# Optimization experiments

Hardware: AMD Instinct MI355X
Metric: run time of the kernel (lower is better)

The kernel has to match this reference:

```python
import jax, jax.numpy as jnp
import numpy as np

N, M, D = 8192, 8192, 1024

def setup_inputs() -> dict:
    key = jax.random.key(0)
    k1, k2 = jax.random.split(key)
    encoder_outputs = jax.random.normal(k1, (N, D), dtype=jnp.float32)
    fact_emb = jax.random.normal(k2, (M, D), dtype=jnp.float32)
    return {"encoder_outputs": encoder_outputs, "fact_emb": fact_emb}

def reference(encoder_outputs, fact_emb):
    # energy: [N, M] = encoder_outputs @ fact_emb^T (unscaled)
    energy = jnp.einsum('nd,md->nm', encoder_outputs, fact_emb)
    weights = jax.nn.softmax(energy, axis=1)          # softmax over facts
    outputs = jnp.einsum('nm,md->nd', weights, fact_emb)
    return (outputs, weights)
```

## Files before the change

kernel.cpp:

```cpp
#include <hip/hip_runtime.h>
#include <hip/hip_bf16.h>
#include <math.h>
#include <stdint.h>

#define N_ROWS 8192
#define M_FACTS 8192
#define D_DIM 1024

typedef __bf16 bf16x8_t __attribute__((ext_vector_type(8)));
typedef __bf16 bf16x4_t __attribute__((ext_vector_type(4)));
typedef float f32x4_t __attribute__((ext_vector_type(4)));

#define BM 128
#define BN 128
#define BK 32
#define PADK 40

__device__ __forceinline__ void gload_lds16(const void* g, void* lds) {
  __builtin_amdgcn_global_load_lds(
      (__attribute__((address_space(1))) void*)(uintptr_t)g,
      (__attribute__((address_space(3))) void*)(uint32_t)(uintptr_t)lds,
      16, 0, 0);
}


__global__ __launch_bounds__(256) void split_hi_lo(const float* __restrict__ X,
                                                   __bf16* __restrict__ H,
                                                   __bf16* __restrict__ L) {
  int i = blockIdx.x * 256 + threadIdx.x;
  float4 v = ((const float4*)X)[i];
  float f[4] = {v.x, v.y, v.z, v.w};
  bf16x4_t h, l;
#pragma unroll
  for (int q = 0; q < 4; q++) {
    __bf16 hh = (__bf16)f[q];
    h[q] = hh;
    l[q] = (__bf16)(f[q] - (float)hh);
  }
  ((bf16x4_t*)H)[i] = h;
  ((bf16x4_t*)L)[i] = l;
}

__global__ __launch_bounds__(256) void transpose_f_bf16(const float* __restrict__ F,
                                                        __bf16* __restrict__ Ft) {
  __shared__ float t[64 * 69];
  const int tid = threadIdx.x;
  const int m0 = blockIdx.x * 64, d0 = blockIdx.y * 64;
#pragma unroll
  for (int p = 0; p < 4; p++) {
    int flat = p * 256 + tid;
    int m = flat >> 4, dq = flat & 15;
    float4 v = *(const float4*)(F + (size_t)(m0 + m) * D_DIM + d0 + dq * 4);
    t[(dq * 4 + 0) * 69 + m] = v.x;
    t[(dq * 4 + 1) * 69 + m] = v.y;
    t[(dq * 4 + 2) * 69 + m] = v.z;
    t[(dq * 4 + 3) * 69 + m] = v.w;
  }
  __syncthreads();
#pragma unroll
  for (int q = 0; q < 2; q++) {
    int id = q * 256 + tid;
    int d = id >> 3, c = id & 7;
    const float* row = t + d * 69 + c * 8;
    bf16x8_t o;
#pragma unroll
    for (int i = 0; i < 8; i++) o[i] = (__bf16)row[i];
    *(bf16x8_t*)(Ft + (size_t)(d0 + d) * M_FACTS + m0 + c * 8) = o;
  }
}

__global__ __launch_bounds__(256) void gemm1_fast(const __bf16* __restrict__ Eh,
                                                  const __bf16* __restrict__ El,
                                                  const __bf16* __restrict__ Fh,
                                                  const __bf16* __restrict__ Fl,
                                                  float* __restrict__ C,
                                                  int row_base) {
  __shared__ __bf16 sAh[BM * BK], sAl[BM * BK], sBh[BN * BK], sBl[BN * BK];
  const int tid = threadIdx.x;
  const int wave = tid >> 6, lane = tid & 63;
  const int row0 = row_base + blockIdx.x * BM, col0 = blockIdx.y * BN;
  const int wm = wave >> 1, wn = wave & 1;
  const int lrow = lane & 15, quad = lane >> 4;

  f32x4_t acc[4][4];
#pragma unroll
  for (int i = 0; i < 4; i++)
#pragma unroll
    for (int j = 0; j < 4; j++) acc[i][j] = (f32x4_t){0.f, 0.f, 0.f, 0.f};

  for (int k0 = 0; k0 < D_DIM; k0 += BK) {
#pragma unroll
    for (int r = 0; r < 2; r++) {
      int c = (r * 4 + wave) * 64 + lane;
      int row = c >> 2;
      int ko = (c & 3) << 3;
      size_t ga = (size_t)(row0 + row) * D_DIM + k0 + ko;
      size_t gb = (size_t)(col0 + row) * D_DIM + k0 + ko;
      gload_lds16(Eh + ga, sAh + c * 8);
      gload_lds16(El + ga, sAl + c * 8);
      gload_lds16(Fh + gb, sBh + c * 8);
      gload_lds16(Fl + gb, sBl + c * 8);
    }
    __syncthreads();

    bf16x8_t ah[4], al[4], bh[4], bl[4];
#pragma unroll
    for (int i = 0; i < 4; i++) {
      int ra = (wm * 64 + i * 16 + lrow) * BK + quad * 8;
      ah[i] = *(const bf16x8_t*)(sAh + ra);
      al[i] = *(const bf16x8_t*)(sAl + ra);
      int rb = (wn * 64 + i * 16 + lrow) * BK + quad * 8;
      bh[i] = *(const bf16x8_t*)(sBh + rb);
      bl[i] = *(const bf16x8_t*)(sBl + rb);
    }
#pragma unroll
    for (int i = 0; i < 4; i++)
#pragma unroll
      for (int j = 0; j < 4; j++) {
        acc[i][j] = __builtin_amdgcn_mfma_f32_16x16x32_bf16(ah[i], bh[j], acc[i][j], 0, 0, 0);
        acc[i][j] = __builtin_amdgcn_mfma_f32_16x16x32_bf16(ah[i], bl[j], acc[i][j], 0, 0, 0);
        acc[i][j] = __builtin_amdgcn_mfma_f32_16x16x32_bf16(al[i], bh[j], acc[i][j], 0, 0, 0);
      }
    __syncthreads();
  }

#pragma unroll
  for (int i = 0; i < 4; i++) {
    int rbase = row0 + wm * 64 + i * 16 + quad * 4;
#pragma unroll
    for (int j = 0; j < 4; j++) {
      int c = col0 + wn * 64 + j * 16 + lrow;
#pragma unroll
      for (int r = 0; r < 4; r++) C[(size_t)(rbase + r) * M_FACTS + c] = acc[i][j][r];
    }
  }
}

__global__ __launch_bounds__(256) void gemm2_reg(const __bf16* __restrict__ Wb,
                                                 const __bf16* __restrict__ Ft,
                                                 float* __restrict__ O,
                                                 int out_row0) {
  __shared__ __bf16 sW[2][BM * BK];
  __shared__ __bf16 sF[2][BN * BK];
  const int tid = threadIdx.x;
  const int wave = tid >> 6, lane = tid & 63;
  const int row0 = blockIdx.x * BM;
  const int col0 = blockIdx.y * BN;
  const int wm = wave >> 1, wn = wave & 1;
  const int lrow = lane & 15, quad = lane >> 4;

  const int id0 = wave * 64 + lane;
  const int r0 = id0 >> 2, c0 = (id0 & 3) << 3;
  const int id1 = id0 + 256;
  const int r1 = id1 >> 2, c1 = (id1 & 3) << 3;

  const __bf16* gW = Wb + (size_t)row0 * M_FACTS;
  const __bf16* gF = Ft + (size_t)col0 * M_FACTS;

  f32x4_t acc[4][4];
#pragma unroll
  for (int i = 0; i < 4; i++)
#pragma unroll
    for (int j = 0; j < 4; j++) acc[i][j] = (f32x4_t){0.f, 0.f, 0.f, 0.f};

  bf16x8_t rW0, rW1, rF0, rF1;
  rW0 = *(const bf16x8_t*)(gW + (size_t)r0 * M_FACTS + c0);
  rW1 = *(const bf16x8_t*)(gW + (size_t)r1 * M_FACTS + c1);
  rF0 = *(const bf16x8_t*)(gF + (size_t)r0 * M_FACTS + c0);
  rF1 = *(const bf16x8_t*)(gF + (size_t)r1 * M_FACTS + c1);
  *(bf16x8_t*)(&sW[0][id0 * 8]) = rW0;
  *(bf16x8_t*)(&sW[0][id1 * 8]) = rW1;
  *(bf16x8_t*)(&sF[0][id0 * 8]) = rF0;
  *(bf16x8_t*)(&sF[0][id1 * 8]) = rF1;
  rW0 = *(const bf16x8_t*)(gW + (size_t)r0 * M_FACTS + BK + c0);
  rW1 = *(const bf16x8_t*)(gW + (size_t)r1 * M_FACTS + BK + c1);
  rF0 = *(const bf16x8_t*)(gF + (size_t)r0 * M_FACTS + BK + c0);
  rF1 = *(const bf16x8_t*)(gF + (size_t)r1 * M_FACTS + BK + c1);
  __syncthreads();

  const int NT = M_FACTS / BK;
  for (int it = 0; it < NT; it++) {
    const int cur = it & 1;
    bf16x8_t a[4], b[4];
#pragma unroll
    for (int i = 0; i < 4; i++) {
      a[i] = *(const bf16x8_t*)(&sW[cur][(wm * 64 + i * 16 + lrow) * BK + quad * 8]);
      b[i] = *(const bf16x8_t*)(&sF[cur][(wn * 64 + i * 16 + lrow) * BK + quad * 8]);
    }
#pragma unroll
    for (int i = 0; i < 4; i++)
#pragma unroll
      for (int j = 0; j < 4; j++)
        acc[i][j] = __builtin_amdgcn_mfma_f32_16x16x32_bf16(a[i], b[j], acc[i][j], 0, 0, 0);

    __syncthreads();
    if (it + 1 < NT) {
      const int nxt = cur ^ 1;
      *(bf16x8_t*)(&sW[nxt][id0 * 8]) = rW0;
      *(bf16x8_t*)(&sW[nxt][id1 * 8]) = rW1;
      *(bf16x8_t*)(&sF[nxt][id0 * 8]) = rF0;
      *(bf16x8_t*)(&sF[nxt][id1 * 8]) = rF1;
      if (it + 2 < NT) {
        const int ko = (it + 2) * BK;
        rW0 = *(const bf16x8_t*)(gW + (size_t)r0 * M_FACTS + ko + c0);
        rW1 = *(const bf16x8_t*)(gW + (size_t)r1 * M_FACTS + ko + c1);
        rF0 = *(const bf16x8_t*)(gF + (size_t)r0 * M_FACTS + ko + c0);
        rF1 = *(const bf16x8_t*)(gF + (size_t)r1 * M_FACTS + ko + c1);
      }
      __syncthreads();
    }
  }

#pragma unroll
  for (int i = 0; i < 4; i++) {
    int rbase = out_row0 + row0 + wm * 64 + i * 16 + quad * 4;
#pragma unroll
    for (int j = 0; j < 4; j++) {
      int c = col0 + wn * 64 + j * 16 + lrow;
#pragma unroll
      for (int r = 0; r < 4; r++) O[(size_t)(rbase + r) * D_DIM + c] = acc[i][j][r];
    }
  }
}

__global__ __launch_bounds__(256) void gemm2_mid(const float* __restrict__ W,
                                                 const __bf16* __restrict__ Ft,
                                                 float* __restrict__ O) {
  __shared__ __bf16 sW[BM * BK], sF[BN * BK];
  const int tid = threadIdx.x;
  const int wave = tid >> 6, lane = tid & 63;
  const int row0 = blockIdx.x * BM, col0 = blockIdx.y * BN;
  const int wm = wave >> 1, wn = wave & 1;
  const int lrow = lane & 15, quad = lane >> 4;

  f32x4_t acc[4][4];
#pragma unroll
  for (int i = 0; i < 4; i++)
#pragma unroll
    for (int j = 0; j < 4; j++) acc[i][j] = (f32x4_t){0.f, 0.f, 0.f, 0.f};

  for (int k0 = 0; k0 < M_FACTS; k0 += BK) {
#pragma unroll
    for (int r = 0; r < 2; r++) {
      int c = (r * 4 + wave) * 64 + lane;
      int row = c >> 2;
      int ko = (c & 3) << 3;
      gload_lds16(Ft + (size_t)(col0 + row) * M_FACTS + k0 + ko, sF + c * 8);
    }
#pragma unroll
    for (int it = 0; it < 4; it++) {
      int flat = it * 256 + tid;
      int r = flat >> 3, q = flat & 7;
      float4 v = *(const float4*)(W + (size_t)(row0 + r) * M_FACTS + k0 + q * 4);
      bf16x4_t h;
      h[0] = (__bf16)v.x;
      h[1] = (__bf16)v.y;
      h[2] = (__bf16)v.z;
      h[3] = (__bf16)v.w;
      *(bf16x4_t*)(sW + r * BK + q * 4) = h;
    }
    __syncthreads();

    bf16x8_t a[4], b[4];
#pragma unroll
    for (int i = 0; i < 4; i++) {
      a[i] = *(const bf16x8_t*)(sW + (wm * 64 + i * 16 + lrow) * BK + quad * 8);
      b[i] = *(const bf16x8_t*)(sF + (wn * 64 + i * 16 + lrow) * BK + quad * 8);
    }
#pragma unroll
    for (int i = 0; i < 4; i++)
#pragma unroll
      for (int j = 0; j < 4; j++)
        acc[i][j] = __builtin_amdgcn_mfma_f32_16x16x32_bf16(a[i], b[j], acc[i][j], 0, 0, 0);
    __syncthreads();
  }

#pragma unroll
  for (int i = 0; i < 4; i++) {
    int rbase = row0 + wm * 64 + i * 16 + quad * 4;
#pragma unroll
    for (int j = 0; j < 4; j++) {
      int c = col0 + wn * 64 + j * 16 + lrow;
#pragma unroll
      for (int r = 0; r < 4; r++) O[(size_t)(rbase + r) * D_DIM + c] = acc[i][j][r];
    }
  }
}

template <bool EMIT_BF16>
__global__ __launch_bounds__(256) void softmax_rows_t(float* __restrict__ W,
                                                      __bf16* __restrict__ Wb) {
  __shared__ float red[8];
  const int tid = threadIdx.x;
  float* p = W + (size_t)blockIdx.x * M_FACTS;

  float4 v[8];
  float mx = -3.4e38f;
#pragma unroll
  for (int i = 0; i < 8; i++) {
    v[i] = *(const float4*)(p + (size_t)(i * 256 + tid) * 4);
    mx = fmaxf(mx, fmaxf(fmaxf(v[i].x, v[i].y), fmaxf(v[i].z, v[i].w)));
  }
#pragma unroll
  for (int off = 32; off >= 1; off >>= 1) mx = fmaxf(mx, __shfl_xor(mx, off));
  const int wave = tid >> 6, lane = tid & 63;
  if (lane == 0) red[wave] = mx;
  __syncthreads();
  mx = fmaxf(fmaxf(red[0], red[1]), fmaxf(red[2], red[3]));

  float s = 0.f;
#pragma unroll
  for (int i = 0; i < 8; i++) {
    v[i].x = __expf(v[i].x - mx);
    v[i].y = __expf(v[i].y - mx);
    v[i].z = __expf(v[i].z - mx);
    v[i].w = __expf(v[i].w - mx);
    s += v[i].x + v[i].y + v[i].z + v[i].w;
  }
#pragma unroll
  for (int off = 32; off >= 1; off >>= 1) s += __shfl_xor(s, off);
  if (lane == 0) red[4 + wave] = s;
  __syncthreads();
  s = red[4] + red[5] + red[6] + red[7];
  float inv = 1.0f / s;
  __bf16* pb = EMIT_BF16 ? (Wb + (size_t)blockIdx.x * M_FACTS) : nullptr;
#pragma unroll
  for (int i = 0; i < 8; i++) {
    v[i].x *= inv;
    v[i].y *= inv;
    v[i].z *= inv;
    v[i].w *= inv;
    *(float4*)(p + (size_t)(i * 256 + tid) * 4) = v[i];
    if (EMIT_BF16) {
      bf16x4_t h;
      h[0] = (__bf16)v[i].x;
      h[1] = (__bf16)v[i].y;
      h[2] = (__bf16)v[i].z;
      h[3] = (__bf16)v[i].w;
      *(bf16x4_t*)(pb + (size_t)(i * 256 + tid) * 4) = h;
    }
  }
}

__global__ __launch_bounds__(256) void gemm1_energy(const float* __restrict__ A,
                                                    const float* __restrict__ B,
                                                    float* __restrict__ C) {
  __shared__ __align__(16) __bf16 sAh[BM * PADK];
  __shared__ __align__(16) __bf16 sAl[BM * PADK];
  __shared__ __align__(16) __bf16 sBh[BN * PADK];
  __shared__ __align__(16) __bf16 sBl[BN * PADK];

  const int tid = threadIdx.x;
  const int row0 = blockIdx.x * BM, col0 = blockIdx.y * BN;
  const int wave = tid >> 6, lane = tid & 63;
  const int wm = wave >> 1, wn = wave & 1;
  const int lrow = lane & 15, quad = lane >> 4;

  f32x4_t acc[4][4];
#pragma unroll
  for (int i = 0; i < 4; i++)
#pragma unroll
    for (int j = 0; j < 4; j++) acc[i][j] = (f32x4_t){0.f, 0.f, 0.f, 0.f};

  for (int k0 = 0; k0 < D_DIM; k0 += BK) {
    __syncthreads();
#pragma unroll
    for (int it = 0; it < 4; it++) {
      int flat = it * 256 + tid;
      int r = flat >> 3, kq = flat & 7;
      float4 va = *(const float4*)(A + (size_t)(row0 + r) * D_DIM + k0 + kq * 4);
      float4 vb = *(const float4*)(B + (size_t)(col0 + r) * D_DIM + k0 + kq * 4);
      float fa[4] = {va.x, va.y, va.z, va.w};
      float fb[4] = {vb.x, vb.y, vb.z, vb.w};
      bf16x4_t ah, al, bh, bl;
#pragma unroll
      for (int q = 0; q < 4; q++) {
        __bf16 h = (__bf16)fa[q];
        ah[q] = h;
        al[q] = (__bf16)(fa[q] - (float)h);
        __bf16 g = (__bf16)fb[q];
        bh[q] = g;
        bl[q] = (__bf16)(fb[q] - (float)g);
      }
      *(bf16x4_t*)(sAh + r * PADK + kq * 4) = ah;
      *(bf16x4_t*)(sAl + r * PADK + kq * 4) = al;
      *(bf16x4_t*)(sBh + r * PADK + kq * 4) = bh;
      *(bf16x4_t*)(sBl + r * PADK + kq * 4) = bl;
    }
    __syncthreads();

    bf16x8_t a_h[4], a_l[4], b_h[4], b_l[4];
#pragma unroll
    for (int i = 0; i < 4; i++) {
      int ra = wm * 64 + i * 16 + lrow;
      a_h[i] = *(const bf16x8_t*)(sAh + ra * PADK + quad * 8);
      a_l[i] = *(const bf16x8_t*)(sAl + ra * PADK + quad * 8);
      int rb = wn * 64 + i * 16 + lrow;
      b_h[i] = *(const bf16x8_t*)(sBh + rb * PADK + quad * 8);
      b_l[i] = *(const bf16x8_t*)(sBl + rb * PADK + quad * 8);
    }
#pragma unroll
    for (int i = 0; i < 4; i++)
#pragma unroll
      for (int j = 0; j < 4; j++) {
        acc[i][j] = __builtin_amdgcn_mfma_f32_16x16x32_bf16(a_h[i], b_h[j], acc[i][j], 0, 0, 0);
        acc[i][j] = __builtin_amdgcn_mfma_f32_16x16x32_bf16(a_h[i], b_l[j], acc[i][j], 0, 0, 0);
        acc[i][j] = __builtin_amdgcn_mfma_f32_16x16x32_bf16(a_l[i], b_h[j], acc[i][j], 0, 0, 0);
      }
  }

#pragma unroll
  for (int i = 0; i < 4; i++) {
    int rbase = row0 + wm * 64 + i * 16 + quad * 4;
#pragma unroll
    for (int j = 0; j < 4; j++) {
      int c = col0 + wn * 64 + j * 16 + lrow;
#pragma unroll
      for (int r = 0; r < 4; r++) C[(size_t)(rbase + r) * M_FACTS + c] = acc[i][j][r];
    }
  }
}

__global__ __launch_bounds__(256) void gemm2_out(const float* __restrict__ W,
                                                 const float* __restrict__ F,
                                                 float* __restrict__ O) {
  __shared__ __align__(16) __bf16 sW[BM * PADK];
  __shared__ __align__(16) __bf16 sFt[BN * PADK];

  const int tid = threadIdx.x;
  const int row0 = blockIdx.x * BM, col0 = blockIdx.y * BN;
  const int wave = tid >> 6, lane = tid & 63;
  const int wm = wave >> 1, wn = wave & 1;
  const int lrow = lane & 15, quad = lane >> 4;

  f32x4_t acc[4][4];
#pragma unroll
  for (int i = 0; i < 4; i++)
#pragma unroll
    for (int j = 0; j < 4; j++) acc[i][j] = (f32x4_t){0.f, 0.f, 0.f, 0.f};

  for (int k0 = 0; k0 < M_FACTS; k0 += BK) {
    __syncthreads();
#pragma unroll
    for (int it = 0; it < 4; it++) {
      int flat = it * 256 + tid;
      int r = flat >> 3, kq = flat & 7;
      float4 v = *(const float4*)(W + (size_t)(row0 + r) * M_FACTS + k0 + kq * 4);
      bf16x4_t h;
      h[0] = (__bf16)v.x;
      h[1] = (__bf16)v.y;
      h[2] = (__bf16)v.z;
      h[3] = (__bf16)v.w;
      *(bf16x4_t*)(sW + r * PADK + kq * 4) = h;
    }
#pragma unroll
    for (int it = 0; it < 4; it++) {
      int flat = it * 256 + tid;
      int m = flat >> 5, dq = flat & 31;
      float4 v = *(const float4*)(F + (size_t)(k0 + m) * D_DIM + col0 + dq * 4);
      sFt[(dq * 4 + 0) * PADK + m] = (__bf16)v.x;
      sFt[(dq * 4 + 1) * PADK + m] = (__bf16)v.y;
      sFt[(dq * 4 + 2) * PADK + m] = (__bf16)v.z;
      sFt[(dq * 4 + 3) * PADK + m] = (__bf16)v.w;
    }
    __syncthreads();

    bf16x8_t a[4], b[4];
#pragma unroll
    for (int i = 0; i < 4; i++) {
      a[i] = *(const bf16x8_t*)(sW + (wm * 64 + i * 16 + lrow) * PADK + quad * 8);
      b[i] = *(const bf16x8_t*)(sFt + (wn * 64 + i * 16 + lrow) * PADK + quad * 8);
    }
#pragma unroll
    for (int i = 0; i < 4; i++)
#pragma unroll
      for (int j = 0; j < 4; j++)
        acc[i][j] = __builtin_amdgcn_mfma_f32_16x16x32_bf16(a[i], b[j], acc[i][j], 0, 0, 0);
  }

#pragma unroll
  for (int i = 0; i < 4; i++) {
    int rbase = row0 + wm * 64 + i * 16 + quad * 4;
#pragma unroll
    for (int j = 0; j < 4; j++) {
      int c = col0 + wn * 64 + j * 16 + lrow;
#pragma unroll
      for (int r = 0; r < 4; r++) O[(size_t)(rbase + r) * D_DIM + c] = acc[i][j][r];
    }
  }
}

extern "C" void kernel_launch(void* const* d_in, const int* in_sizes, int n_in,
                              void* d_out, int out_size, void* d_ws, size_t ws_size,
                              hipStream_t stream) {
  const float* E = (const float*)d_in[0];
  const float* F = (const float*)d_in[1];
  float* outputs = (float*)d_out;
  float* weights = (float*)d_out + (size_t)N_ROWS * D_DIM;

  const size_t MB = 1ull << 20;
  char* ws = (char*)d_ws;

  const bool t1 = ws_size >= 144 * MB;
  const bool t2 = !t1 && ws_size >= 80 * MB;
  const bool hasFtOnly = !t1 && !t2 && ws_size >= 16 * MB;

  if (t1 || t2) {
    __bf16* Ft = (__bf16*)(ws + 0 * MB);
    __bf16* Eh = (__bf16*)(ws + 16 * MB);
    __bf16* El = (__bf16*)(ws + 32 * MB);
    __bf16* Fh = (__bf16*)(ws + 48 * MB);
    __bf16* Fl = (__bf16*)(ws + 64 * MB);
    __bf16* Wb = (__bf16*)(ws + 16 * MB);

    transpose_f_bf16<<<dim3(M_FACTS / 64, D_DIM / 64), 256, 0, stream>>>(F, Ft);
    split_hi_lo<<<dim3((N_ROWS * D_DIM) / 1024), 256, 0, stream>>>(E, Eh, El);
    split_hi_lo<<<dim3((M_FACTS * D_DIM) / 1024), 256, 0, stream>>>(F, Fh, Fl);
    for (int b = 0; b < 2; b++) {
      gemm1_fast<<<dim3(32, M_FACTS / BN), 256, 0, stream>>>(Eh, El, Fh, Fl, weights,
                                                             b * (N_ROWS / 2));
    }

    if (t1) {
      softmax_rows_t<true><<<dim3(N_ROWS), 256, 0, stream>>>(weights, Wb);
      gemm2_reg<<<dim3(N_ROWS / BM, D_DIM / BN), 256, 0, stream>>>(Wb, Ft, outputs, 0);
    } else {
      const int HALF = N_ROWS / 2;
      for (int h = 0; h < 2; h++) {
        float* Wchunk = weights + (size_t)h * HALF * M_FACTS;
        softmax_rows_t<true><<<dim3(HALF), 256, 0, stream>>>(Wchunk, Wb);
        gemm2_reg<<<dim3(HALF / BM, D_DIM / BN), 256, 0, stream>>>(Wb, Ft, outputs, h * HALF);
      }
    }
  } else {
    __bf16* Ft = (__bf16*)ws;
    if (hasFtOnly) {
      transpose_f_bf16<<<dim3(M_FACTS / 64, D_DIM / 64), 256, 0, stream>>>(F, Ft);
    }
    gemm1_energy<<<dim3(N_ROWS / BM, M_FACTS / BN), 256, 0, stream>>>(E, F, weights);
    softmax_rows_t<false><<<dim3(N_ROWS), 256, 0, stream>>>(weights, nullptr);
    if (hasFtOnly) {
      gemm2_mid<<<dim3(N_ROWS / BM, D_DIM / BN), 256, 0, stream>>>(weights, Ft, outputs);
    } else {
      gemm2_out<<<dim3(N_ROWS / BM, D_DIM / BN), 256, 0, stream>>>(weights, F, outputs);
    }
  }
}
```

Measured before the change: 970.3 us.

## Split-K second GEMM with atomic accumulation and merge gemm1 launches

Replaces the register-pipelined second GEMM with a simpler LDS-staged kernel that splits the 8192-long reduction into two halves across a z grid dimension. Partial results are combined with atomic adds into a pre-zeroed output, and a new zero-fill kernel runs first. The two half-size gemm1 launches are merged into one full launch. This doubles the block count for gemm2 (64x8 was only 512 blocks) to improve occupancy, at the cost of atomic traffic, an extra zeroing pass, and losing the double-buffered pipeline.

```diff
diff --git a/kernel.cpp b/kernel.cpp
--- a/kernel.cpp
+++ b/kernel.cpp
@@ -67,6 +67,11 @@
     for (int i = 0; i < 8; i++) o[i] = (__bf16)row[i];
     *(bf16x8_t*)(Ft + (size_t)(d0 + d) * M_FACTS + m0 + c * 8) = o;
   }
+}
+
+__global__ __launch_bounds__(256) void zero_out(float* __restrict__ O) {
+  size_t i = (size_t)blockIdx.x * 256 + threadIdx.x;
+  ((float4*)O)[i] = (float4){0.f, 0.f, 0.f, 0.f};
 }
 
 __global__ __launch_bounds__(256) void gemm1_fast(const __bf16* __restrict__ Eh,
@@ -132,6 +137,67 @@
       int c = col0 + wn * 64 + j * 16 + lrow;
 #pragma unroll
       for (int r = 0; r < 4; r++) C[(size_t)(rbase + r) * M_FACTS + c] = acc[i][j][r];
+    }
+  }
+}
+
+__global__ __launch_bounds__(256, 4) void gemm2_lds(const __bf16* __restrict__ Wb,
+                                                    const __bf16* __restrict__ Ft,
+                                                    float* __restrict__ O) {
+  __shared__ __bf16 sW[BM * BK], sF[BN * BK];
+  const int tid = threadIdx.x;
+  const int wave = tid >> 6, lane = tid & 63;
+  const int row0 = blockIdx.x * BM;
+  const int col0 = blockIdx.y * BN;
+  const int kbase = blockIdx.z * (M_FACTS / 2);
+  const int wm = wave >> 1, wn = wave & 1;
+  const int lrow = lane & 15, quad = lane >> 4;
+
+  const int c0 = wave * 64 + lane;
+  const int c1 = c0 + 256;
+  const int rA0 = c0 >> 2, kA0 = (c0 & 3) << 3;
+  const int rA1 = c1 >> 2, kA1 = (c1 & 3) << 3;
+  const __bf16* pW0 = Wb + (size_t)(row0 + rA0) * M_FACTS + kbase + kA0;
+  const __bf16* pW1 = Wb + (size_t)(row0 + rA1) * M_FACTS + kbase + kA1;
+  const __bf16* pF0 = Ft + (size_t)(col0 + rA0) * M_FACTS + kbase + kA0;
+  const __bf16* pF1 = Ft + (size_t)(col0 + rA1) * M_FACTS + kbase + kA1;
+
+  f32x4_t acc[4][4];
+#pragma unroll
+  for (int i = 0; i < 4; i++)
+#pragma unroll
+    for (int j = 0; j < 4; j++) acc[i][j] = (f32x4_t){0.f, 0.f, 0.f, 0.f};
+
+  for (int k0 = 0; k0 < M_FACTS / 2; k0 += BK) {
+    gload_lds16(pW0 + k0, sW + c0 * 8);
+    gload_lds16(pW1 + k0, sW + c1 * 8);
+    gload_lds16(pF0 + k0, sF + c0 * 8);
+    gload_lds16(pF1 + k0, sF + c1 * 8);
+    __syncthreads();
+
+    bf16x8_t a[4], b[4];
+#pragma unroll
+    for (int i = 0; i < 4; i++) {
+      a[i] = *(const bf16x8_t*)(sW + (wm * 64 + i * 16 + lrow) * BK + quad * 8);
+      b[i] = *(const bf16x8_t*)(sF + (wn * 64 + i * 16 + lrow) * BK + quad * 8);
+    }
+#pragma unroll
+    for (int i = 0; i < 4; i++)
+#pragma unroll
+      for (int j = 0; j < 4; j++)
+        acc[i][j] = __builtin_amdgcn_mfma_f32_16x16x32_bf16(a[i], b[j], acc[i][j], 0, 0, 0);
+    __syncthreads();
+  }
+
+#pragma unroll
+  for (int i = 0; i < 4; i++) {
+    int rbase = row0 + wm * 64 + i * 16 + quad * 4;
+#pragma unroll
+    for (int j = 0; j < 4; j++) {
+      int c = col0 + wn * 64 + j * 16 + lrow;
+#pragma unroll
+      for (int r = 0; r < 4; r++)
+        unsafeAtomicAdd(&O[(size_t)(rbase + r) * D_DIM + c], acc[i][j][r]);
     }
   }
 }
@@ -516,14 +582,15 @@
     transpose_f_bf16<<<dim3(M_FACTS / 64, D_DIM / 64), 256, 0, stream>>>(F, Ft);
     split_hi_lo<<<dim3((N_ROWS * D_DIM) / 1024), 256, 0, stream>>>(E, Eh, El);
     split_hi_lo<<<dim3((M_FACTS * D_DIM) / 1024), 256, 0, stream>>>(F, Fh, Fl);
-    for (int b = 0; b < 2; b++) {
-      gemm1_fast<<<dim3(32, M_FACTS / BN), 256, 0, stream>>>(Eh, El, Fh, Fl, weights,
-                                                             b * (N_ROWS / 2));
-    }
+    if (t1) {
+      zero_out<<<dim3((N_ROWS * D_DIM) / 1024), 256, 0, stream>>>(outputs);
+    }
+    gemm1_fast<<<dim3(N_ROWS / BM, M_FACTS / BN), 256, 0, stream>>>(Eh, El, Fh, Fl,
+                                                                    weights, 0);
 
     if (t1) {
       softmax_rows_t<true><<<dim3(N_ROWS), 256, 0, stream>>>(weights, Wb);
-      gemm2_reg<<<dim3(N_ROWS / BM, D_DIM / BN), 256, 0, stream>>>(Wb, Ft, outputs, 0);
+      gemm2_lds<<<dim3(N_ROWS / BM, D_DIM / BN, 2), 256, 0, stream>>>(Wb, Ft, outputs);
     } else {
       const int HALF = N_ROWS / 2;
       for (int h = 0; h < 2; h++) {
```

New measurement: 998.9 us. 1.03x slower.

## Use concatenated hi/lo bf16 operands with 256x256 double-buffered GEMM and split-K

Applied to the files above, without the earlier changes.

On the large-workspace path, the bf16x3 split is recast as a single GEMM over K=3072. E is stored as [hi, lo, hi] and F as [hi, hi, lo], so one new 256x256-tile, 512-thread, LDS double-buffered MFMA kernel with XOR swizzle computes the energy. The second GEMM reuses that kernel with split-K over 2 slices and accumulates with atomics into a pre-zeroed output, which adds blocks for the small N x D output. This is meant to raise tile reuse and MFMA utilisation over the previous 128x128 kernels, at the cost of an extra zeroing pass, atomic-add nondeterminism and higher LDS and register pressure.

```diff
diff --git a/kernel.cpp b/kernel.cpp
--- a/kernel.cpp
+++ b/kernel.cpp
@@ -39,6 +39,44 @@
   }
   ((bf16x4_t*)H)[i] = h;
   ((bf16x4_t*)L)[i] = l;
+}
+
+__global__ __launch_bounds__(256) void split_concat_E(const float* __restrict__ X,
+                                                      __bf16* __restrict__ A2) {
+  int idx = blockIdx.x * 256 + threadIdx.x;
+  int n = idx >> 8, d4 = idx & 255;
+  float4 v = ((const float4*)X)[idx];
+  float f[4] = {v.x, v.y, v.z, v.w};
+  bf16x4_t h, l;
+#pragma unroll
+  for (int q = 0; q < 4; q++) {
+    __bf16 hh = (__bf16)f[q];
+    h[q] = hh;
+    l[q] = (__bf16)(f[q] - (float)hh);
+  }
+  size_t base = (size_t)n * 3072 + d4 * 4;
+  *(bf16x4_t*)(A2 + base) = h;
+  *(bf16x4_t*)(A2 + base + 1024) = l;
+  *(bf16x4_t*)(A2 + base + 2048) = h;
+}
+
+__global__ __launch_bounds__(256) void split_concat_F(const float* __restrict__ X,
+                                                      __bf16* __restrict__ B2) {
+  int idx = blockIdx.x * 256 + threadIdx.x;
+  int m = idx >> 8, d4 = idx & 255;
+  float4 v = ((const float4*)X)[idx];
+  float f[4] = {v.x, v.y, v.z, v.w};
+  bf16x4_t h, l;
+#pragma unroll
+  for (int q = 0; q < 4; q++) {
+    __bf16 hh = (__bf16)f[q];
+    h[q] = hh;
+    l[q] = (__bf16)(f[q] - (float)hh);
+  }
+  size_t base = (size_t)m * 3072 + d4 * 4;
+  *(bf16x4_t*)(B2 + base) = h;
+  *(bf16x4_t*)(B2 + base + 1024) = h;
+  *(bf16x4_t*)(B2 + base + 2048) = l;
 }
 
 __global__ __launch_bounds__(256) void transpose_f_bf16(const float* __restrict__ F,
@@ -66,6 +104,132 @@
 #pragma unroll
     for (int i = 0; i < 8; i++) o[i] = (__bf16)row[i];
     *(bf16x8_t*)(Ft + (size_t)(d0 + d) * M_FACTS + m0 + c * 8) = o;
+  }
+}
+
+__global__ __launch_bounds__(256) void zero_out(float* __restrict__ O) {
+  size_t i = (size_t)blockIdx.x * 256 + threadIdx.x;
+  ((float4*)O)[i] = (float4){0.f, 0.f, 0.f, 0.f};
+}
+
+template <bool ATOMIC>
+__global__ __launch_bounds__(512, 2) void gemm_8ph(const __bf16* __restrict__ A,
+                                                   const __bf16* __restrict__ B,
+                                                   float* __restrict__ C,
+                                                   int K, int lda, int ldb, int ldc) {
+  __shared__ __bf16 sA[2][256 * 64];
+  __shared__ __bf16 sB[2][256 * 64];
+  const int tid = threadIdx.x;
+  const int wave = tid >> 6, lane = tid & 63;
+  const int wm = wave >> 2;
+  const int wn = wave & 3;
+  const int lrow = lane & 15, quad = lane >> 4;
+  const int row0 = blockIdx.x * 256;
+  const int col0 = blockIdx.y * 256;
+  const int kbase = blockIdx.z * K;
+
+  const int g0 = tid, g1 = tid + 512;
+  const int sr0 = g0 >> 3, sq0 = g0 & 7;
+  const int sr1 = g1 >> 3, sq1 = g1 & 7;
+  const int so0 = (sq0 ^ (sr0 & 7)) << 3;
+  const int so1 = (sq1 ^ (sr1 & 7)) << 3;
+
+  f32x4_t acc[8][4];
+#pragma unroll
+  for (int i = 0; i < 8; i++)
+#pragma unroll
+    for (int j = 0; j < 4; j++) acc[i][j] = (f32x4_t){0.f, 0.f, 0.f, 0.f};
+
+  auto STAGE = [&](int buf, int kt, int h) {
+    const int ko = kbase + kt * 64;
+    if (h < 2) {
+      gload_lds16(A + (size_t)(row0 + h * 128 + sr0) * lda + ko + so0,
+                  &sA[buf][h * 8192 + g0 * 8]);
+      gload_lds16(A + (size_t)(row0 + h * 128 + sr1) * lda + ko + so1,
+                  &sA[buf][h * 8192 + g1 * 8]);
+    } else {
+      const int hh = h - 2;
+      gload_lds16(B + (size_t)(col0 + hh * 128 + sr0) * ldb + ko + so0,
+                  &sB[buf][hh * 8192 + g0 * 8]);
+      gload_lds16(B + (size_t)(col0 + hh * 128 + sr1) * ldb + ko + so1,
+                  &sB[buf][hh * 8192 + g1 * 8]);
+    }
+  };
+
+  const int nkt = K >> 6;
+
+#pragma unroll
+  for (int h = 0; h < 4; h++) STAGE(0, 0, h);
+  asm volatile("s_waitcnt vmcnt(0)" ::: "memory");
+  __builtin_amdgcn_s_barrier();
+  __builtin_amdgcn_sched_barrier(0);
+
+  for (int t = 0; t < nkt; ++t) {
+    const int cur = t & 1;
+    const __bf16* lA = &sA[cur][0];
+    const __bf16* lB = &sB[cur][0];
+    const bool pf = (t + 1 < nkt);
+
+#pragma unroll
+    for (int p = 0; p < 4; ++p) {
+      const int rhalf = p >> 1, chalf = p & 1;
+      bf16x8_t af[4][2], bfr[2][2];
+#pragma unroll
+      for (int rf = 0; rf < 4; ++rf) {
+        const int r = rhalf * 64 + rf * 16 + lrow;
+#pragma unroll
+        for (int ks = 0; ks < 2; ++ks)
+          af[rf][ks] = *(const bf16x8_t*)(lA + wm * 8192 + r * 64 +
+                                          (((ks * 4 + quad) ^ (r & 7)) << 3));
+      }
+#pragma unroll
+      for (int j = 0; j < 2; ++j) {
+        const int col = wn * 64 + chalf * 32 + j * 16 + lrow;
+        const int bh = col >> 7, c = col & 127;
+#pragma unroll
+        for (int ks = 0; ks < 2; ++ks)
+          bfr[j][ks] = *(const bf16x8_t*)(lB + bh * 8192 + c * 64 +
+                                          (((ks * 4 + quad) ^ (c & 7)) << 3));
+      }
+      if (pf) {
+        if (p == 0) { STAGE(cur ^ 1, t + 1, 0); STAGE(cur ^ 1, t + 1, 1); }
+        if (p == 1) { STAGE(cur ^ 1, t + 1, 2); STAGE(cur ^ 1, t + 1, 3); }
+      }
+      __builtin_amdgcn_s_setprio(1);
+#pragma unroll
+      for (int rf = 0; rf < 4; ++rf)
+#pragma unroll
+        for (int j = 0; j < 2; ++j)
+#pragma unroll
+          for (int ks = 0; ks < 2; ++ks)
+            acc[rhalf * 4 + rf][chalf * 2 + j] = __builtin_amdgcn_mfma_f32_16x16x32_bf16(
+                af[rf][ks], bfr[j][ks], acc[rhalf * 4 + rf][chalf * 2 + j], 0, 0, 0);
+      __builtin_amdgcn_s_setprio(0);
+      if (p < 3) {
+        __builtin_amdgcn_sched_barrier(0);
+        __builtin_amdgcn_s_barrier();
+        __builtin_amdgcn_sched_barrier(0);
+      }
+    }
+    asm volatile("s_waitcnt vmcnt(0)" ::: "memory");
+    __builtin_amdgcn_s_barrier();
+    __builtin_amdgcn_sched_barrier(0);
+  }
+
+#pragma unroll
+  for (int i = 0; i < 8; ++i) {
+    const int rbase = row0 + wm * 128 + (i >> 2) * 64 + (i & 3) * 16 + quad * 4;
+#pragma unroll
+    for (int j = 0; j < 4; ++j) {
+      const int c = col0 + wn * 64 + (j >> 1) * 32 + (j & 1) * 16 + lrow;
+#pragma unroll
+      for (int r = 0; r < 4; ++r) {
+        if (ATOMIC)
+          unsafeAtomicAdd(&C[(size_t)(rbase + r) * ldc + c], acc[i][j][r]);
+        else
+          C[(size_t)(rbase + r) * ldc + c] = acc[i][j][r];
+      }
+    }
   }
 }
 
@@ -505,7 +669,25 @@
   const bool t2 = !t1 && ws_size >= 80 * MB;
   const bool hasFtOnly = !t1 && !t2 && ws_size >= 16 * MB;
 
-  if (t1 || t2) {
+  if (t1) {
+    __bf16* Ft = (__bf16*)(ws + 0 * MB);
+    __bf16* A2 = (__bf16*)(ws + 16 * MB);
+    __bf16* B2 = (__bf16*)(ws + 64 * MB);
+    __bf16* Wb = (__bf16*)(ws + 16 * MB);
+
+    transpose_f_bf16<<<dim3(M_FACTS / 64, D_DIM / 64), 256, 0, stream>>>(F, Ft);
+    split_concat_E<<<dim3((N_ROWS * D_DIM) / 1024), 256, 0, stream>>>(E, A2);
+    split_concat_F<<<dim3((M_FACTS * D_DIM) / 1024), 256, 0, stream>>>(F, B2);
+    zero_out<<<dim3((N_ROWS * D_DIM) / 1024), 256, 0, stream>>>(outputs);
+
+    gemm_8ph<false><<<dim3(N_ROWS / 256, M_FACTS / 256), 512, 0, stream>>>(
+        A2, B2, weights, 3072, 3072, 3072, M_FACTS);
+
+    softmax_rows_t<true><<<dim3(N_ROWS), 256, 0, stream>>>(weights, Wb);
+
+    gemm_8ph<true><<<dim3(N_ROWS / 256, D_DIM / 256, 2), 512, 0, stream>>>(
+        Wb, Ft, outputs, M_FACTS / 2, M_FACTS, M_FACTS, D_DIM);
+  } else if (t2) {
     __bf16* Ft = (__bf16*)(ws + 0 * MB);
     __bf16* Eh = (__bf16*)(ws + 16 * MB);
     __bf16* El = (__bf16*)(ws + 32 * MB);
@@ -516,21 +698,13 @@
     transpose_f_bf16<<<dim3(M_FACTS / 64, D_DIM / 64), 256, 0, stream>>>(F, Ft);
     split_hi_lo<<<dim3((N_ROWS * D_DIM) / 1024), 256, 0, stream>>>(E, Eh, El);
     split_hi_lo<<<dim3((M_FACTS * D_DIM) / 1024), 256, 0, stream>>>(F, Fh, Fl);
-    for (int b = 0; b < 2; b++) {
-      gemm1_fast<<<dim3(32, M_FACTS / BN), 256, 0, stream>>>(Eh, El, Fh, Fl, weights,
-                                                             b * (N_ROWS / 2));
-    }
-
-    if (t1) {
-      softmax_rows_t<true><<<dim3(N_ROWS), 256, 0, stream>>>(weights, Wb);
-      gemm2_reg<<<dim3(N_ROWS / BM, D_DIM / BN), 256, 0, stream>>>(Wb, Ft, outputs, 0);
-    } else {
-      const int HALF = N_ROWS / 2;
-      for (int h = 0; h < 2; h++) {
-        float* Wchunk = weights + (size_t)h * HALF * M_FACTS;
-        softmax_rows_t<true><<<dim3(HALF), 256, 0, stream>>>(Wchunk, Wb);
-        gemm2_reg<<<dim3(HALF / BM, D_DIM / BN), 256, 0, stream>>>(Wb, Ft, outputs, h * HALF);
-      }
+    gemm1_fast<<<dim3(N_ROWS / BM, M_FACTS / BN), 256, 0, stream>>>(Eh, El, Fh, Fl,
+                                                                    weights, 0);
+    const int HALF = N_ROWS / 2;
+    for (int h = 0; h < 2; h++) {
+      float* Wchunk = weights + (size_t)h * HALF * M_FACTS;
+      softmax_rows_t<true><<<dim3(HALF), 256, 0, stream>>>(Wchunk, Wb);
+      gemm2_reg<<<dim3(HALF / BM, D_DIM / BN), 256, 0, stream>>>(Wb, Ft, outputs, h * HALF);
     }
   } else {
     __bf16* Ft = (__bf16*)ws;
```

Result: faster. 927.2 us (-4.4%).
